# Optimization experiments

Hardware: AMD Instinct MI355X
Metric: run time of the kernel (lower is better)

## Reference

```python
import jax, jax.numpy as jnp
import numpy as np

# Dimensions
B2, T, C = 400, 120, 128          # x: ((B*V), T, C)
V = 25                            # num_point (skeleton joints)
NH_A = 3                          # adjacency heads (A.shape[0])
HEADS, DH = 8, 64                 # attention heads, dim_head
INNER = HEADS * DH                # 512
QKV_C = INNER * 3                 # 1536 = GCN out_channels
EPS = 1e-5                        # torch BatchNorm2d default eps


def setup_inputs() -> dict:
    key = jax.random.key(0)
    ks = jax.random.split(key, 12)
    z = lambda *s: jnp.zeros(s, jnp.float32)
    o = lambda *s: jnp.ones(s, jnp.float32)
    return {
        "x": jax.random.normal(ks[0], (B2, T, C), jnp.float32),
        # GCN shared topology (num_head, V, V)
        "A": jax.random.normal(ks[1], (NH_A, V, V), jnp.float32) * 0.2,
        # per-head 1x1 conv weights/biases (stacked)
        "conv_w": jax.random.normal(ks[2], (NH_A, QKV_C, C), jnp.float32) * 0.02,
        "conv_b": jax.random.normal(ks[3], (NH_A, QKV_C), jnp.float32) * 0.01,
        # main BatchNorm2d (eval mode, running stats)
        "bn_gamma": jax.random.uniform(ks[4], (QKV_C,), jnp.float32, 0.5, 1.5),
        "bn_beta": z(QKV_C),
        "bn_mean": z(QKV_C),
        "bn_var": o(QKV_C),
        # down path: 1x1 conv + BatchNorm2d (in_c != out_c)
        "down_w": jax.random.normal(ks[5], (QKV_C, C), jnp.float32) * 0.02,
        "down_b": z(QKV_C),
        "dbn_gamma": jax.random.uniform(ks[6], (QKV_C,), jnp.float32, 0.5, 1.5),
        "dbn_beta": z(QKV_C),
        "dbn_mean": z(QKV_C),
        "dbn_var": o(QKV_C),
        # to_out Linear(inner_dim -> dim)
        "out_w": jax.random.normal(ks[7], (C, INNER), jnp.float32) * 0.02,
        "out_b": z(C),
    }


def _bn_eval(y, gamma, beta, mean, var):
    # y: (b, o, t, v); BN over channel axis 1, eval mode
    inv = gamma / jnp.sqrt(var + EPS)
    return y * inv[None, :, None, None] + (beta - mean * inv)[None, :, None, None]


def reference(x, A, conv_w, conv_b, bn_gamma, bn_beta, bn_mean, bn_var,
              down_w, down_b, dbn_gamma, dbn_beta, dbn_mean, dbn_var,
              out_w, out_b):
    B = B2 // V
    # '(b v) t c -> b c t v'
    x4 = x.reshape(B, V, T, C).transpose(0, 3, 2, 1)  # (b, c, t, v)

    # ---- GCN projection: sum_h Conv1x1_h(A_h @ x) ----
    z = jnp.einsum('hvu,bctu->bhctv', A, x4)                    # (b,h,c,t,v)
    y = jnp.einsum('hoc,bhctv->botv', conv_w, z)                # (b,O,t,v)
    y = y + conv_b.sum(0)[None, :, None, None]
    y = _bn_eval(y, bn_gamma, bn_beta, bn_mean, bn_var)

    d = jnp.einsum('oc,bctv->botv', down_w, x4) + down_b[None, :, None, None]
    d = _bn_eval(d, dbn_gamma, dbn_beta, dbn_mean, dbn_var)

    y = jax.nn.relu(y + d)                                      # (b,O,t,v)

    # ---- attention over time per (batch*joint) row ----
    qkv = y.transpose(0, 3, 2, 1).reshape(B2, T, QKV_C)         # '(b v) t c'
    q, k, v = jnp.split(qkv, 3, axis=-1)
    split_heads = lambda t: t.reshape(B2, T, HEADS, DH).transpose(0, 2, 1, 3)
    q, k, v = split_heads(q), split_heads(k), split_heads(v)

    dots = jnp.einsum('bhid,bhjd->bhij', q, k) * (DH ** -0.5)
    mask = jnp.tril(jnp.ones((T, T), bool))                     # causal mask
    dots = jnp.where(mask[None, None], dots, -jnp.inf)
    attn = jax.nn.softmax(dots, axis=-1)                        # (B2,H,T,T)

    o = jnp.einsum('bhij,bhjd->bhid', attn, v)
    o = o.transpose(0, 2, 1, 3).reshape(B2, T, INNER)
    out = o @ out_w.T + out_b                                   # (B2,T,C)
    return out, attn
```

## Files before the change

### kernel.cpp

```cpp
#include <hip/hip_runtime.h>


typedef __bf16 bf16;
typedef __bf16 bf16x8 __attribute__((ext_vector_type(8)));
typedef __bf16 bf16x4 __attribute__((ext_vector_type(4)));
typedef float  f32x4  __attribute__((ext_vector_type(4)));
typedef __attribute__((address_space(1))) const void* gptr1;
typedef __attribute__((address_space(3))) void*       lptr3;

#define GLL16(g, l) __builtin_amdgcn_global_load_lds((gptr1)(g), (lptr3)(l), 16, 0, 0)
#define MFMA16(a, b, c) __builtin_amdgcn_mfma_f32_16x16x32_bf16(a, b, c, 0, 0, 0)

__global__ __launch_bounds__(256) void build_weights(
    const float* __restrict__ conv_w, const float* __restrict__ conv_b,
    const float* __restrict__ g1, const float* __restrict__ be1,
    const float* __restrict__ mu1, const float* __restrict__ va1,
    const float* __restrict__ down_w, const float* __restrict__ down_b,
    const float* __restrict__ g2, const float* __restrict__ be2,
    const float* __restrict__ mu2, const float* __restrict__ va2,
    const float* __restrict__ out_w,
    bf16* __restrict__ wcat, bf16* __restrict__ wout, float* __restrict__ bias)
{
    int idx = blockIdx.x * 256 + threadIdx.x;
    if (idx < 1536 * 512) {
        int o = idx >> 9, k = idx & 511;
        float s, w;
        if (k < 384) {
            int h = k >> 7, c = k & 127;
            s = g1[o] * rsqrtf(va1[o] + 1e-5f);
            w = conv_w[(h * 1536 + o) * 128 + c];
        } else {
            s = g2[o] * rsqrtf(va2[o] + 1e-5f);
            w = down_w[o * 128 + (k - 384)];
        }
        wcat[idx] = (bf16)(w * s);
    }
    int i2 = idx - 1536 * 512;
    if (i2 >= 0 && i2 < 128 * 512) wout[i2] = (bf16)out_w[i2];
    int i3 = idx - (1536 * 512 + 128 * 512);
    if (i3 >= 0 && i3 < 1536) {
        int o = i3;
        float s1 = g1[o] * rsqrtf(va1[o] + 1e-5f);
        float s2 = g2[o] * rsqrtf(va2[o] + 1e-5f);
        float cb = conv_b[o] + conv_b[1536 + o] + conv_b[2 * 1536 + o];
        bias[o] = cb * s1 + be1[o] - mu1[o] * s1
                + down_b[o] * s2 + be2[o] - mu2[o] * s2;
    }
}

__global__ __launch_bounds__(256) void transform(
    const float* __restrict__ x, const float* __restrict__ A,
    bf16* __restrict__ zt)
{
    __shared__ float xs[25][128];
    const int tid = threadIdx.x;
    const int bt = blockIdx.x;
    const int b = bt / 120, t = bt - b * 120;
    for (int i = tid; i < 25 * 128; i += 256) {
        int u = i >> 7, c = i & 127;
        xs[u][c] = x[((size_t)(b * 25 + u) * 120 + t) * 128 + c];
    }
    __syncthreads();
    const int c = tid & 127, g = tid >> 7;
    float xr[25];
    #pragma unroll
    for (int u = 0; u < 25; u++) xr[u] = xs[u][c];
    for (int idx = g; idx < 75; idx += 2) {
        int h = idx / 25, v = idx - h * 25;
        const float* Ap = A + (h * 25 + v) * 25;
        float acc = 0.f;
        #pragma unroll
        for (int u = 0; u < 25; u++) acc += Ap[u] * xr[u];
        zt[((size_t)(b * 25 + v) * 120 + t) * 512 + h * 128 + c] = (bf16)acc;
    }
    for (int v = g; v < 25; v += 2)
        zt[((size_t)(b * 25 + v) * 120 + t) * 512 + 384 + c] = (bf16)xs[v][c];
}

__global__ __launch_bounds__(256) void gemm_qkv(
    const bf16* __restrict__ wcat, const bf16* __restrict__ zt,
    const float* __restrict__ bias,
    bf16* __restrict__ qg, bf16* __restrict__ kg, bf16* __restrict__ vtg)
{
    __shared__ __align__(16) char smem[65536];
    const int tid = threadIdx.x, lane = tid & 63, wv = tid >> 6;
    const int wrow = wv >> 1, wcol = wv & 1;
    const int NB = 4500, q8 = NB >> 3, r8 = NB & 7;
    const int xcd = blockIdx.x & 7, sidx = blockIdx.x >> 3;
    const int vid = (xcd < r8 ? xcd * (q8 + 1) : r8 * (q8 + 1) + (xcd - r8) * q8) + sidx;
    const int mt = vid % 12, nt = vid / 12;
    const int colb = lane & 15, rg = lane >> 4;

    f32x4 acc[4][4];
    #pragma unroll
    for (int i = 0; i < 4; i++)
        #pragma unroll
        for (int j = 0; j < 4; j++) acc[i][j] = (f32x4){0.f, 0.f, 0.f, 0.f};

    const char* gA = (const char*)wcat + (size_t)mt * 128 * 1024;
    const char* gB = (const char*)zt + (size_t)nt * 128 * 1024;

    int aoff[4][2], boff[4][2];
    #pragma unroll
    for (int m = 0; m < 4; m++)
        #pragma unroll
        for (int kk = 0; kk < 2; kk++) {
            int swz = (rg * 16 + kk * 64) ^ ((colb & 7) << 4);
            aoff[m][kk] = (wrow * 64 + m * 16 + colb) * 128 + swz;
            boff[m][kk] = (wcol * 64 + m * 16 + colb) * 128 + swz;
        }

    #define STG(kt, bsel) do {                                                  \
        char* As_ = smem + (bsel) * 32768; char* Bs_ = As_ + 16384;             \
        _Pragma("unroll")                                                       \
        for (int j = 0; j < 4; j++) {                                           \
            int c = j * 256 + tid;                                              \
            int r = c >> 3, sl = (c & 7) ^ (r & 7);                             \
            GLL16(gA + (size_t)r * 1024 + (kt) * 128 + sl * 16, As_ + c * 16);  \
            GLL16(gB + (size_t)r * 1024 + (kt) * 128 + sl * 16, Bs_ + c * 16);  \
        } } while (0)

    STG(0, 0);
    asm volatile("s_waitcnt vmcnt(0)" ::: "memory");
    __builtin_amdgcn_s_barrier();
    for (int p = 0; p < 8; p++) {
        const char* As = smem + (p & 1) * 32768;
        const char* Bs = As + 16384;
        if (p < 7) STG(p + 1, (p + 1) & 1);
        bf16x8 af[4][2], bfr[4][2];
        #pragma unroll
        for (int m = 0; m < 4; m++)
            #pragma unroll
            for (int kk = 0; kk < 2; kk++) {
                af[m][kk]  = *(const bf16x8*)(As + aoff[m][kk]);
                bfr[m][kk] = *(const bf16x8*)(Bs + boff[m][kk]);
            }
        __builtin_amdgcn_s_setprio(1);
        #pragma unroll
        for (int m = 0; m < 4; m++)
            #pragma unroll
            for (int n = 0; n < 4; n++)
                #pragma unroll
                for (int kk = 0; kk < 2; kk++)
                    acc[m][n] = MFMA16(af[m][kk], bfr[n][kk], acc[m][n]);
        __builtin_amdgcn_s_setprio(0);
        asm volatile("s_waitcnt vmcnt(0)" ::: "memory");
        __builtin_amdgcn_s_barrier();
    }
    __builtin_amdgcn_sched_barrier(0);

    const int mtb = mt * 128, ntb = nt * 128;
    const int which = mtb >> 9;

    if (which < 2) {
        bf16* Lt = (bf16*)smem;
        const float qs = (which == 0) ? 0.125f : 1.0f;
        #pragma unroll
        for (int m = 0; m < 4; m++) {
            int o0 = wrow * 64 + m * 16 + rg * 4;
            float b0 = bias[mtb + o0 + 0], b1 = bias[mtb + o0 + 1];
            float b2 = bias[mtb + o0 + 2], b3 = bias[mtb + o0 + 3];
            #pragma unroll
            for (int nn = 0; nn < 4; nn++) {
                int n_ = wcol * 64 + nn * 16 + colb;
                bf16x4 pk;
                pk[0] = (bf16)(fmaxf(acc[m][nn][0] + b0, 0.f) * qs);
                pk[1] = (bf16)(fmaxf(acc[m][nn][1] + b1, 0.f) * qs);
                pk[2] = (bf16)(fmaxf(acc[m][nn][2] + b2, 0.f) * qs);
                pk[3] = (bf16)(fmaxf(acc[m][nn][3] + b3, 0.f) * qs);
                *(bf16x4*)((char*)Lt + n_ * 256 + ((o0 * 2) ^ ((n_ & 7) << 4))) = pk;
            }
        }
        __syncthreads();
        bf16* dst = (which == 0) ? qg : kg;
        #pragma unroll
        for (int i = 0; i < 8; i++) {
            int ch = i * 256 + tid;
            int n_ = ch >> 4, c16 = ch & 15;
            int ng = ntb + n_;
            int grp = ng / 120, t = ng - grp * 120;
            int o = mtb + c16 * 8;
            int hd = (o >> 6) & 7, dd0 = o & 63;
            bf16x8 vv = *(const bf16x8*)((const char*)Lt + n_ * 256 +
                                         ((c16 * 16) ^ ((n_ & 7) << 4)));
            *(bf16x8*)(dst + ((size_t)(grp * 8 + hd) * 120 + t) * 64 + dd0) = vv;
        }
    } else {
        #pragma unroll
        for (int m = 0; m < 4; m++) {
            #pragma unroll
            for (int reg = 0; reg < 4; reg++) {
                int o = mtb + wrow * 64 + m * 16 + rg * 4 + reg;
                float bo = bias[o];
                int hd = (o >> 6) & 7, dd = o & 63;
                #pragma unroll
                for (int nn = 0; nn < 4; nn++) {
                    int n = ntb + wcol * 64 + nn * 16 + colb;
                    int grp = n / 120, t = n - grp * 120;
                    float val = fmaxf(acc[m][nn][reg] + bo, 0.f);
                    vtg[((size_t)(grp * 8 + hd) * 64 + dd) * 128 + t] = (bf16)val;
                }
            }
        }
    }
    #undef STG
}

__global__ __launch_bounds__(256) void attn_k(
    const bf16* __restrict__ qg, const bf16* __restrict__ kg,
    const bf16* __restrict__ vtg, float* __restrict__ attn_out,
    bf16* __restrict__ og)
{
    __shared__ __align__(16) char sm[49152];
    char* Vt = sm;
    char* Ks = sm + 16384;
    char* Ps = sm + 16384;
    const int tid = threadIdx.x, lane = tid & 63, wv = tid >> 6;
    const int bh = blockIdx.x;
    const int colb = lane & 15, rg = lane >> 4;

    const char* ksrc = (const char*)kg + (size_t)bh * 15360;
    const char* vsrc = (const char*)vtg + (size_t)bh * 16384;
    #pragma unroll
    for (int is = 0; is < 4; is++) {
        int cb = is * 256 + wv * 64;
        if (cb < 960) {
            int bb = (cb + lane) * 16;
            int row = bb >> 7;
            int gsrc = (bb & ~127) | ((bb & 127) ^ ((row & 7) << 4));
            GLL16(ksrc + gsrc, Ks + cb * 16);
        }
    }
    const char* qsrc = (const char*)qg + (size_t)bh * 15360;
    bf16x8 qf[2][2];
    #pragma unroll
    for (int kk = 0; kk < 2; kk++)
        #pragma unroll
        for (int m = 0; m < 2; m++) {
            int row = wv * 32 + m * 16 + colb;
            qf[kk][m] = *(const bf16x8*)(qsrc + (size_t)row * 128 + rg * 16 + kk * 64);
        }
    #pragma unroll
    for (int is = 0; is < 4; is++) {
        int cb = is * 256 + wv * 64;
        int bb = (cb + lane) * 16;
        int row = bb >> 8;
        int gsrc = (bb & ~255) | ((bb & 255) ^ ((row & 7) << 4));
        GLL16(vsrc + gsrc, Vt + cb * 16);
    }
    asm volatile("s_waitcnt vmcnt(4)" ::: "memory");
    __builtin_amdgcn_s_barrier();
    if (tid < 64) {
        f32x4 z = {0.f, 0.f, 0.f, 0.f};
        int r = 120 + (tid >> 3), off = (tid & 7) * 16;
        *(f32x4*)(Ks + r * 128 + off) = z;
    }
    asm volatile("s_waitcnt lgkmcnt(0)" ::: "memory");
    __builtin_amdgcn_s_barrier();

    f32x4 accs[2][8];
    #pragma unroll
    for (int m = 0; m < 2; m++)
        #pragma unroll
        for (int ct = 0; ct < 8; ct++) accs[m][ct] = (f32x4){0.f, 0.f, 0.f, 0.f};
    #pragma unroll
    for (int kk = 0; kk < 2; kk++) {
        #pragma unroll
        for (int ct = 0; ct < 8; ct++) {
            int rk = ct * 16 + colb;
            int byo = rk * 128 + ((rg * 16 + kk * 64) ^ ((rk & 7) << 4));
            bf16x8 bk = *(const bf16x8*)(Ks + byo);
            accs[0][ct] = MFMA16(qf[kk][0], bk, accs[0][ct]);
            accs[1][ct] = MFMA16(qf[kk][1], bk, accs[1][ct]);
        }
    }
    asm volatile("s_waitcnt vmcnt(0)" ::: "memory");
    __builtin_amdgcn_s_barrier();
    if (tid >= 64 && tid < 128) {
        int d = tid - 64;
        f32x4 z = {0.f, 0.f, 0.f, 0.f};
        *(f32x4*)(Vt + d * 256 + (240 ^ ((d & 7) << 4))) = z;
    }

    const int rqb = wv * 32;
    #pragma unroll
    for (int m = 0; m < 2; m++) {
        #pragma unroll
        for (int reg = 0; reg < 4; reg++) {
            int t_q = rqb + m * 16 + rg * 4 + reg;
            float s[8], mx = -1e30f;
            #pragma unroll
            for (int ct = 0; ct < 8; ct++) {
                int col = ct * 16 + colb;
                bool valid = (col <= t_q) && (col < 120);
                s[ct] = valid ? accs[m][ct][reg] : -1e30f;
                mx = fmaxf(mx, s[ct]);
            }
            #pragma unroll
            for (int d = 1; d < 16; d <<= 1) mx = fmaxf(mx, __shfl_xor(mx, d, 64));
            float p[8], sum = 0.f;
            #pragma unroll
            for (int ct = 0; ct < 8; ct++) {
                p[ct] = (s[ct] > -1e29f) ? __expf(s[ct] - mx) : 0.f;
                sum += p[ct];
            }
            #pragma unroll
            for (int d = 1; d < 16; d <<= 1) sum += __shfl_xor(sum, d, 64);
            float inv = 1.f / sum;
            #pragma unroll
            for (int ct = 0; ct < 8; ct++) {
                int col = ct * 16 + colb;
                int byo = t_q * 256 + ((col * 2) ^ ((t_q & 7) << 4));
                *(bf16*)(Ps + byo) = (bf16)(p[ct] * inv);
            }
        }
    }
    asm volatile("s_waitcnt lgkmcnt(0)" ::: "memory");
    __builtin_amdgcn_s_barrier();

    f32x4 acco[2][4];
    #pragma unroll
    for (int m = 0; m < 2; m++)
        #pragma unroll
        for (int dt = 0; dt < 4; dt++) acco[m][dt] = (f32x4){0.f, 0.f, 0.f, 0.f};
    for (int kk = 0; kk <= wv; kk++) {
        bf16x8 ap[2];
        #pragma unroll
        for (int m = 0; m < 2; m++) {
            int row = rqb + m * 16 + colb;
            int byo = row * 256 + ((rg * 16 + kk * 64) ^ ((row & 7) << 4));
            ap[m] = *(const bf16x8*)(Ps + byo);
        }
        #pragma unroll
        for (int dt = 0; dt < 4; dt++) {
            int rd = dt * 16 + colb;
            int byo = rd * 256 + ((rg * 16 + kk * 64) ^ ((rd & 7) << 4));
            bf16x8 bv = *(const bf16x8*)(Vt + byo);
            acco[0][dt] = MFMA16(ap[0], bv, acco[0][dt]);
            acco[1][dt] = MFMA16(ap[1], bv, acco[1][dt]);
        }
    }

    {
        float* attn_base = attn_out + (size_t)bh * 14400;
        #pragma unroll
        for (int i = 0; i < 15; i++) {
            int chunk = i * 256 + tid;
            if (chunk < 3600) {
                int r = chunk / 30, c4 = chunk - r * 30;
                int byo = r * 256 + ((c4 * 8) ^ ((r & 7) << 4));
                bf16x4 pv4 = *(const bf16x4*)(Ps + byo);
                f32x4 o4 = { (float)pv4[0], (float)pv4[1],
                             (float)pv4[2], (float)pv4[3] };
                *(f32x4*)(attn_base + chunk * 4) = o4;
            }
        }
    }

    const int b2 = bh >> 3, h = bh & 7;
    #pragma unroll
    for (int m = 0; m < 2; m++)
        #pragma unroll
        for (int dt = 0; dt < 4; dt++)
            #pragma unroll
            for (int reg = 0; reg < 4; reg++) {
                int t = rqb + m * 16 + rg * 4 + reg;
                if (t < 120) {
                    int dfull = h * 64 + dt * 16 + colb;
                    og[((size_t)b2 * 120 + t) * 512 + dfull] = (bf16)acco[m][dt][reg];
                }
            }
}

__global__ __launch_bounds__(256) void gemm_out_k(
    const bf16* __restrict__ og, const bf16* __restrict__ wout,
    const float* __restrict__ outb, float* __restrict__ out)
{
    __shared__ __align__(16) char smem[65536];
    const int tid = threadIdx.x, lane = tid & 63, wv = tid >> 6;
    const int wrow = wv >> 1, wcol = wv & 1;
    const int nt = blockIdx.x;
    const int colb = lane & 15, rg = lane >> 4;

    f32x4 acc[4][4];
    #pragma unroll
    for (int i = 0; i < 4; i++)
        #pragma unroll
        for (int j = 0; j < 4; j++) acc[i][j] = (f32x4){0.f, 0.f, 0.f, 0.f};

    const char* gA = (const char*)og + (size_t)nt * 128 * 1024;
    const char* gB = (const char*)wout;

    int aoff[4][2], boff[4][2];
    #pragma unroll
    for (int m = 0; m < 4; m++)
        #pragma unroll
        for (int kk = 0; kk < 2; kk++) {
            int swz = (rg * 16 + kk * 64) ^ ((colb & 7) << 4);
            aoff[m][kk] = (wrow * 64 + m * 16 + colb) * 128 + swz;
            boff[m][kk] = (wcol * 64 + m * 16 + colb) * 128 + swz;
        }

    #define STG_O(kt, bsel) do {                                                \
        char* As_ = smem + (bsel) * 32768; char* Bs_ = As_ + 16384;             \
        _Pragma("unroll")                                                       \
        for (int j = 0; j < 4; j++) {                                           \
            int c = j * 256 + tid;                                              \
            int r = c >> 3, sl = (c & 7) ^ (r & 7);                             \
            GLL16(gA + (size_t)r * 1024 + (kt) * 128 + sl * 16, As_ + c * 16);  \
            GLL16(gB + (size_t)r * 1024 + (kt) * 128 + sl * 16, Bs_ + c * 16);  \
        } } while (0)

    STG_O(0, 0);
    asm volatile("s_waitcnt vmcnt(0)" ::: "memory");
    __builtin_amdgcn_s_barrier();
    for (int p = 0; p < 8; p++) {
        const char* As = smem + (p & 1) * 32768;
        const char* Bs = As + 16384;
        if (p < 7) STG_O(p + 1, (p + 1) & 1);
        bf16x8 af[4][2], bfr[4][2];
        #pragma unroll
        for (int m = 0; m < 4; m++)
            #pragma unroll
            for (int kk = 0; kk < 2; kk++) {
                af[m][kk]  = *(const bf16x8*)(As + aoff[m][kk]);
                bfr[m][kk] = *(const bf16x8*)(Bs + boff[m][kk]);
            }
        __builtin_amdgcn_s_setprio(1);
        #pragma unroll
        for (int m = 0; m < 4; m++)
            #pragma unroll
            for (int n = 0; n < 4; n++)
                #pragma unroll
                for (int kk = 0; kk < 2; kk++)
                    acc[m][n] = MFMA16(af[m][kk], bfr[n][kk], acc[m][n]);
        __builtin_amdgcn_s_setprio(0);
        asm volatile("s_waitcnt vmcnt(0)" ::: "memory");
        __builtin_amdgcn_s_barrier();
    }
    __builtin_amdgcn_sched_barrier(0);

    const int rbase = nt * 128 + wrow * 64;
    #pragma unroll
    for (int m = 0; m < 4; m++)
        #pragma unroll
        for (int reg = 0; reg < 4; reg++) {
            int r = rbase + m * 16 + rg * 4 + reg;
            #pragma unroll
            for (int nn = 0; nn < 4; nn++) {
                int c = wcol * 64 + nn * 16 + colb;
                out[(size_t)r * 128 + c] = acc[m][nn][reg] + outb[c];
            }
        }
    #undef STG_O
}

extern "C" void kernel_launch(void* const* d_in, const int* in_sizes, int n_in,
                              void* d_out, int out_size, void* d_ws, size_t ws_size,
                              hipStream_t stream)
{
    (void)in_sizes; (void)n_in; (void)out_size; (void)ws_size;
    const float* x      = (const float*)d_in[0];
    const float* A      = (const float*)d_in[1];
    const float* conv_w = (const float*)d_in[2];
    const float* conv_b = (const float*)d_in[3];
    const float* bn_g   = (const float*)d_in[4];
    const float* bn_b   = (const float*)d_in[5];
    const float* bn_m   = (const float*)d_in[6];
    const float* bn_v   = (const float*)d_in[7];
    const float* dw     = (const float*)d_in[8];
    const float* db     = (const float*)d_in[9];
    const float* dg     = (const float*)d_in[10];
    const float* dbb    = (const float*)d_in[11];
    const float* dm     = (const float*)d_in[12];
    const float* dvv    = (const float*)d_in[13];
    const float* out_w  = (const float*)d_in[14];
    const float* out_b  = (const float*)d_in[15];

    char* ws = (char*)d_ws;
    const size_t OFF_WCAT = 0;
    const size_t OFF_WOUT = 1572864;
    const size_t OFF_BIAS = 1703936;
    const size_t OFF_ZT   = 1710080;
    const size_t OFF_Q    = 50862080;
    const size_t OFF_K    = 100014080;
    const size_t OFF_VT   = 149166080;
    const size_t OFF_O    = OFF_ZT;

    bf16*  wcat = (bf16*)(ws + OFF_WCAT);
    bf16*  wout = (bf16*)(ws + OFF_WOUT);
    float* bias = (float*)(ws + OFF_BIAS);
    bf16*  zt   = (bf16*)(ws + OFF_ZT);
    bf16*  qg   = (bf16*)(ws + OFF_Q);
    bf16*  kg   = (bf16*)(ws + OFF_K);
    bf16*  vtg  = (bf16*)(ws + OFF_VT);
    bf16*  og   = (bf16*)(ws + OFF_O);
    float* outp = (float*)d_out;
    float* attn = outp + 6144000;

    build_weights<<<3334, 256, 0, stream>>>(conv_w, conv_b, bn_g, bn_b, bn_m, bn_v,
                                            dw, db, dg, dbb, dm, dvv, out_w,
                                            wcat, wout, bias);
    transform<<<1920, 256, 0, stream>>>(x, A, zt);
    gemm_qkv<<<4500, 256, 0, stream>>>(wcat, zt, bias, qg, kg, vtg);
    attn_k<<<3200, 256, 0, stream>>>(qg, kg, vtg, attn, og);
    gemm_out_k<<<375, 256, 0, stream>>>(og, wout, out_b, outp);
}
```

Before: 262.9 us.

## Widen QKV GEMM tile to 128x256 with BK=32 and padded zero rows

```diff
diff --git a/kernel.cpp b/kernel.cpp
--- a/kernel.cpp
+++ b/kernel.cpp
@@ -19,7 +19,8 @@
     const float* __restrict__ g2, const float* __restrict__ be2,
     const float* __restrict__ mu2, const float* __restrict__ va2,
     const float* __restrict__ out_w,
-    bf16* __restrict__ wcat, bf16* __restrict__ wout, float* __restrict__ bias)
+    bf16* __restrict__ wcat, bf16* __restrict__ wout, float* __restrict__ bias,
+    bf16* __restrict__ zt)
 {
     int idx = blockIdx.x * 256 + threadIdx.x;
     if (idx < 1536 * 512) {
@@ -46,6 +47,9 @@
         bias[o] = cb * s1 + be1[o] - mu1[o] * s1
                 + down_b[o] * s2 + be2[o] - mu2[o] * s2;
     }
+    int i4 = idx - (1536 * 512 + 128 * 512 + 1536);
+    if (i4 >= 0 && i4 < 128 * 512)
+        zt[(size_t)48000 * 512 + i4] = (bf16)0.f;
 }
 
 __global__ __launch_bounds__(256) void transform(
@@ -82,128 +86,153 @@
     const float* __restrict__ bias,
     bf16* __restrict__ qg, bf16* __restrict__ kg, bf16* __restrict__ vtg)
 {
-    __shared__ __align__(16) char smem[65536];
+    __shared__ __align__(16) char smem[49152];
     const int tid = threadIdx.x, lane = tid & 63, wv = tid >> 6;
     const int wrow = wv >> 1, wcol = wv & 1;
-    const int NB = 4500, q8 = NB >> 3, r8 = NB & 7;
-    const int xcd = blockIdx.x & 7, sidx = blockIdx.x >> 3;
-    const int vid = (xcd < r8 ? xcd * (q8 + 1) : r8 * (q8 + 1) + (xcd - r8) * q8) + sidx;
-    const int mt = vid % 12, nt = vid / 12;
+    const int vid = (blockIdx.x & 7) * 282 + (blockIdx.x >> 3);
+    const int mt = vid % 12, nt2 = vid / 12;
+    const int mtb = mt * 128, ntb = nt2 * 256;
     const int colb = lane & 15, rg = lane >> 4;
 
-    f32x4 acc[4][4];
+    f32x4 acc0[4][4], acc1[4][4];
     #pragma unroll
     for (int i = 0; i < 4; i++)
         #pragma unroll
-        for (int j = 0; j < 4; j++) acc[i][j] = (f32x4){0.f, 0.f, 0.f, 0.f};
-
-    const char* gA = (const char*)wcat + (size_t)mt * 128 * 1024;
-    const char* gB = (const char*)zt + (size_t)nt * 128 * 1024;
-
-    int aoff[4][2], boff[4][2];
-    #pragma unroll
-    for (int m = 0; m < 4; m++)
-        #pragma unroll
-        for (int kk = 0; kk < 2; kk++) {
-            int swz = (rg * 16 + kk * 64) ^ ((colb & 7) << 4);
-            aoff[m][kk] = (wrow * 64 + m * 16 + colb) * 128 + swz;
-            boff[m][kk] = (wcol * 64 + m * 16 + colb) * 128 + swz;
-        }
+        for (int j = 0; j < 4; j++) {
+            acc0[i][j] = (f32x4){0.f, 0.f, 0.f, 0.f};
+            acc1[i][j] = (f32x4){0.f, 0.f, 0.f, 0.f};
+        }
+
+    const char* gA  = (const char*)wcat + (size_t)mtb * 1024;
+    const char* gB0 = (const char*)zt + (size_t)ntb * 1024;
+    const char* gB1 = (const char*)zt + (size_t)(ntb + 128) * 1024;
+
+    const int rgs = rg ^ ((colb >> 1) & 3);
+    int aoff[4], boff[4];
+    #pragma unroll
+    for (int m = 0; m < 4; m++) {
+        aoff[m] = (wrow * 64 + m * 16 + colb) * 64 + rgs * 16;
+        boff[m] = (wcol * 64 + m * 16 + colb) * 64 + rgs * 16;
+    }
 
     #define STG(kt, bsel) do {                                                  \
-        char* As_ = smem + (bsel) * 32768; char* Bs_ = As_ + 16384;             \
+        char* Bse = smem + (bsel) * 24576;                                      \
         _Pragma("unroll")                                                       \
-        for (int j = 0; j < 4; j++) {                                           \
+        for (int j = 0; j < 2; j++) {                                           \
             int c = j * 256 + tid;                                              \
-            int r = c >> 3, sl = (c & 7) ^ (r & 7);                             \
-            GLL16(gA + (size_t)r * 1024 + (kt) * 128 + sl * 16, As_ + c * 16);  \
-            GLL16(gB + (size_t)r * 1024 + (kt) * 128 + sl * 16, Bs_ + c * 16);  \
+            int r = c >> 2, sl = (c & 3) ^ ((c >> 3) & 3);                      \
+            size_t go = (size_t)r * 1024 + (kt) * 64 + sl * 16;                 \
+            GLL16(gA + go, Bse + c * 16);                                       \
+            GLL16(gB0 + go, Bse + 8192 + c * 16);                               \
+            GLL16(gB1 + go, Bse + 16384 + c * 16);                              \
         } } while (0)
 
     STG(0, 0);
     asm volatile("s_waitcnt vmcnt(0)" ::: "memory");
     __builtin_amdgcn_s_barrier();
-    for (int p = 0; p < 8; p++) {
-        const char* As = smem + (p & 1) * 32768;
-        const char* Bs = As + 16384;
-        if (p < 7) STG(p + 1, (p + 1) & 1);
-        bf16x8 af[4][2], bfr[4][2];
+    for (int p = 0; p < 16; p++) {
+        const char* As  = smem + (p & 1) * 24576;
+        const char* Bs0 = As + 8192;
+        const char* Bs1 = As + 16384;
+        if (p < 15) STG(p + 1, (p + 1) & 1);
+        bf16x8 af[4], bfr[4];
         #pragma unroll
         for (int m = 0; m < 4; m++)
-            #pragma unroll
-            for (int kk = 0; kk < 2; kk++) {
-                af[m][kk]  = *(const bf16x8*)(As + aoff[m][kk]);
-                bfr[m][kk] = *(const bf16x8*)(Bs + boff[m][kk]);
-            }
+            af[m] = *(const bf16x8*)(As + aoff[m]);
+        #pragma unroll
+        for (int n = 0; n < 4; n++)
+            bfr[n] = *(const bf16x8*)(Bs0 + boff[n]);
         __builtin_amdgcn_s_setprio(1);
         #pragma unroll
         for (int m = 0; m < 4; m++)
             #pragma unroll
             for (int n = 0; n < 4; n++)
-                #pragma unroll
-                for (int kk = 0; kk < 2; kk++)
-                    acc[m][n] = MFMA16(af[m][kk], bfr[n][kk], acc[m][n]);
+                acc0[m][n] = MFMA16(af[m], bfr[n], acc0[m][n]);
+        __builtin_amdgcn_s_setprio(0);
+        #pragma unroll
+        for (int n = 0; n < 4; n++)
+            bfr[n] = *(const bf16x8*)(Bs1 + boff[n]);
+        __builtin_amdgcn_s_setprio(1);
+        #pragma unroll
+        for (int m = 0; m < 4; m++)
+            #pragma unroll
+            for (int n = 0; n < 4; n++)
+                acc1[m][n] = MFMA16(af[m], bfr[n], acc1[m][n]);
         __builtin_amdgcn_s_setprio(0);
         asm volatile("s_waitcnt vmcnt(0)" ::: "memory");
         __builtin_amdgcn_s_barrier();
     }
     __builtin_amdgcn_sched_barrier(0);
 
-    const int mtb = mt * 128, ntb = nt * 128;
     const int which = mtb >> 9;
+    const float qs = (which == 0) ? 0.125f : 1.0f;
+
+    #define EPILOGUE_QK(ACC, SUB) do {                                          \
+        bf16* Lt = (bf16*)smem;                    \
+        _Pragma("unroll")                                                       \
+        for (int m = 0; m < 4; m++) {                                           \
+            int o0 = wrow * 64 + m * 16 + rg * 4;                               \
+            float b0 = bias[mtb + o0 + 0], b1 = bias[mtb + o0 + 1];             \
+            float b2 = bias[mtb + o0 + 2], b3 = bias[mtb + o0 + 3];             \
+            _Pragma("unroll")                                                   \
+            for (int nn = 0; nn < 4; nn++) {                                    \
+                int n_ = wcol * 64 + nn * 16 + colb;                            \
+                bf16x4 pk;                                                      \
+                pk[0] = (bf16)(fmaxf(ACC[m][nn][0] + b0, 0.f) * qs);            \
+                pk[1] = (bf16)(fmaxf(ACC[m][nn][1] + b1, 0.f) * qs);            \
+                pk[2] = (bf16)(fmaxf(ACC[m][nn][2] + b2, 0.f) * qs);            \
+                pk[3] = (bf16)(fmaxf(ACC[m][nn][3] + b3, 0.f) * qs);            \
+                *(bf16x4*)((char*)Lt + n_ * 256 + ((o0 * 2) ^ ((n_ & 7) << 4))) = pk; \
+            }                                                                   \
+        }                                                                       \
+        __syncthreads();                                                        \
+        bf16* dst = (which == 0) ? qg : kg;                                     \
+        _Pragma("unroll")                                                       \
+        for (int i = 0; i < 8; i++) {                                           \
+            int ch = i * 256 + tid;                                             \
+            int n_ = ch >> 4, c16 = ch & 15;                                    \
+            int ng = ntb + (SUB) * 128 + n_;                                    \
+            if (ng < 48000) {                                                   \
+                int grp = ng / 120, t = ng - grp * 120;                         \
+                int o = mtb + c16 * 8;                                          \
+                int hd = (o >> 6) & 7, dd0 = o & 63;                            \
+                bf16x8 vv = *(const bf16x8*)((const char*)Lt + n_ * 256 +       \
+                                             ((c16 * 16) ^ ((n_ & 7) << 4)));   \
+                *(bf16x8*)(dst + ((size_t)(grp * 8 + hd) * 120 + t) * 64 + dd0) = vv; \
+            }                                                                   \
+        } } while (0)
+
+    #define EPILOGUE_V(ACC, SUB) do {                                           \
+        _Pragma("unroll")                                                       \
+        for (int m = 0; m < 4; m++) {                                           \
+            _Pragma("unroll")                                                   \
+            for (int reg = 0; reg < 4; reg++) {                                 \
+                int o = mtb + wrow * 64 + m * 16 + rg * 4 + reg;                \
+                float bo = bias[o];                                             \
+                int hd = (o >> 6) & 7, dd = o & 63;                             \
+                _Pragma("unroll")                                               \
+                for (int nn = 0; nn < 4; nn++) {                                \
+                    int n = ntb + (SUB) * 128 + wcol * 64 + nn * 16 + colb;     \
+                    if (n < 48000) {                                            \
+                        int grp = n / 120, t = n - grp * 120;                   \
+                        float val = fmaxf(ACC[m][nn][reg] + bo, 0.f);           \
+                        vtg[((size_t)(grp * 8 + hd) * 64 + dd) * 128 + t] = (bf16)val; \
+                    }                                                           \
+                }                                                               \
+            }                                                                   \
+        } } while (0)
 
     if (which < 2) {
-        bf16* Lt = (bf16*)smem;
-        const float qs = (which == 0) ? 0.125f : 1.0f;
-        #pragma unroll
-        for (int m = 0; m < 4; m++) {
-            int o0 = wrow * 64 + m * 16 + rg * 4;
-            float b0 = bias[mtb + o0 + 0], b1 = bias[mtb + o0 + 1];
-            float b2 = bias[mtb + o0 + 2], b3 = bias[mtb + o0 + 3];
-            #pragma unroll
-            for (int nn = 0; nn < 4; nn++) {
-                int n_ = wcol * 64 + nn * 16 + colb;
-                bf16x4 pk;
-                pk[0] = (bf16)(fmaxf(acc[m][nn][0] + b0, 0.f) * qs);
-                pk[1] = (bf16)(fmaxf(acc[m][nn][1] + b1, 0.f) * qs);
-                pk[2] = (bf16)(fmaxf(acc[m][nn][2] + b2, 0.f) * qs);
-                pk[3] = (bf16)(fmaxf(acc[m][nn][3] + b3, 0.f) * qs);
-                *(bf16x4*)((char*)Lt + n_ * 256 + ((o0 * 2) ^ ((n_ & 7) << 4))) = pk;
-            }
-        }
+        EPILOGUE_QK(acc0, 0);
         __syncthreads();
-        bf16* dst = (which == 0) ? qg : kg;
-        #pragma unroll
-        for (int i = 0; i < 8; i++) {
-            int ch = i * 256 + tid;
-            int n_ = ch >> 4, c16 = ch & 15;
-            int ng = ntb + n_;
-            int grp = ng / 120, t = ng - grp * 120;
-            int o = mtb + c16 * 8;
-            int hd = (o >> 6) & 7, dd0 = o & 63;
-            bf16x8 vv = *(const bf16x8*)((const char*)Lt + n_ * 256 +
-                                         ((c16 * 16) ^ ((n_ & 7) << 4)));
-            *(bf16x8*)(dst + ((size_t)(grp * 8 + hd) * 120 + t) * 64 + dd0) = vv;
-        }
+        EPILOGUE_QK(acc1, 1);
     } else {
-        #pragma unroll
-        for (int m = 0; m < 4; m++) {
-            #pragma unroll
-            for (int reg = 0; reg < 4; reg++) {
-                int o = mtb + wrow * 64 + m * 16 + rg * 4 + reg;
-                float bo = bias[o];
-                int hd = (o >> 6) & 7, dd = o & 63;
-                #pragma unroll
-                for (int nn = 0; nn < 4; nn++) {
-                    int n = ntb + wcol * 64 + nn * 16 + colb;
-                    int grp = n / 120, t = n - grp * 120;
-                    float val = fmaxf(acc[m][nn][reg] + bo, 0.f);
-                    vtg[((size_t)(grp * 8 + hd) * 64 + dd) * 128 + t] = (bf16)val;
-                }
-            }
-        }
+        EPILOGUE_V(acc0, 0);
+        EPILOGUE_V(acc1, 1);
     }
     #undef STG
+    #undef EPILOGUE_QK
+    #undef EPILOGUE_V
 }
 
 __global__ __launch_bounds__(256) void attn_k(
@@ -482,9 +511,9 @@
     const size_t OFF_WOUT = 1572864;
     const size_t OFF_BIAS = 1703936;
     const size_t OFF_ZT   = 1710080;
-    const size_t OFF_Q    = 50862080;
-    const size_t OFF_K    = 100014080;
-    const size_t OFF_VT   = 149166080;
+    const size_t OFF_Q    = 50993152;
+    const size_t OFF_K    = 100145152;
+    const size_t OFF_VT   = 149297152;
     const size_t OFF_O    = OFF_ZT;
 
     bf16*  wcat = (bf16*)(ws + OFF_WCAT);
@@ -498,11 +527,11 @@
     float* outp = (float*)d_out;
     float* attn = outp + 6144000;
 
-    build_weights<<<3334, 256, 0, stream>>>(conv_w, conv_b, bn_g, bn_b, bn_m, bn_v,
+    build_weights<<<3590, 256, 0, stream>>>(conv_w, conv_b, bn_g, bn_b, bn_m, bn_v,
                                             dw, db, dg, dbb, dm, dvv, out_w,
-                                            wcat, wout, bias);
+                                            wcat, wout, bias, zt);
     transform<<<1920, 256, 0, stream>>>(x, A, zt);
-    gemm_qkv<<<4500, 256, 0, stream>>>(wcat, zt, bias, qg, kg, vtg);
+    gemm_qkv<<<2256, 256, 0, stream>>>(wcat, zt, bias, qg, kg, vtg);
     attn_k<<<3200, 256, 0, stream>>>(qg, kg, vtg, attn, og);
     gemm_out_k<<<375, 256, 0, stream>>>(og, wout, out_b, outp);
 }
```

After: 384.5 us. +46.2%, slower.

## Enlarge QKV GEMM tile to 256x128 with 512 threads and triple-buffered K=32 pipeline

Applied to the files above, without the earlier changes.

```diff
diff --git a/kernel.cpp b/kernel.cpp
--- a/kernel.cpp
+++ b/kernel.cpp
@@ -77,18 +77,18 @@
         zt[((size_t)(b * 25 + v) * 120 + t) * 512 + 384 + c] = (bf16)xs[v][c];
 }
 
-__global__ __launch_bounds__(256) void gemm_qkv(
+__global__ __launch_bounds__(512, 4) void gemm_qkv(
     const bf16* __restrict__ wcat, const bf16* __restrict__ zt,
     const float* __restrict__ bias,
     bf16* __restrict__ qg, bf16* __restrict__ kg, bf16* __restrict__ vtg)
 {
-    __shared__ __align__(16) char smem[65536];
+    __shared__ __align__(16) char smem[73728];
     const int tid = threadIdx.x, lane = tid & 63, wv = tid >> 6;
     const int wrow = wv >> 1, wcol = wv & 1;
-    const int NB = 4500, q8 = NB >> 3, r8 = NB & 7;
     const int xcd = blockIdx.x & 7, sidx = blockIdx.x >> 3;
-    const int vid = (xcd < r8 ? xcd * (q8 + 1) : r8 * (q8 + 1) + (xcd - r8) * q8) + sidx;
-    const int mt = vid % 12, nt = vid / 12;
+    const int vid = (xcd < 2 ? xcd * 282 : 564 + (xcd - 2) * 281) + sidx;
+    const int mt = vid % 6, nt = vid / 6;
+    const int mtb = mt * 256, ntb = nt * 128;
     const int colb = lane & 15, rg = lane >> 4;
 
     f32x4 acc[4][4];
@@ -97,60 +97,61 @@
         #pragma unroll
         for (int j = 0; j < 4; j++) acc[i][j] = (f32x4){0.f, 0.f, 0.f, 0.f};
 
-    const char* gA = (const char*)wcat + (size_t)mt * 128 * 1024;
-    const char* gB = (const char*)zt + (size_t)nt * 128 * 1024;
-
-    int aoff[4][2], boff[4][2];
-    #pragma unroll
-    for (int m = 0; m < 4; m++)
-        #pragma unroll
-        for (int kk = 0; kk < 2; kk++) {
-            int swz = (rg * 16 + kk * 64) ^ ((colb & 7) << 4);
-            aoff[m][kk] = (wrow * 64 + m * 16 + colb) * 128 + swz;
-            boff[m][kk] = (wcol * 64 + m * 16 + colb) * 128 + swz;
-        }
+    const char* gA = (const char*)wcat + (size_t)mtb * 1024;
+    const char* gB = (const char*)zt + (size_t)ntb * 1024;
+
+    const int rgs = rg ^ ((colb >> 1) & 3);
+    int aoff[4], boff[4];
+    #pragma unroll
+    for (int m = 0; m < 4; m++) {
+        aoff[m] = (wrow * 64 + m * 16 + colb) * 64 + rgs * 16;
+        boff[m] = (wcol * 64 + m * 16 + colb) * 64 + rgs * 16;
+    }
 
     #define STG(kt, bsel) do {                                                  \
-        char* As_ = smem + (bsel) * 32768; char* Bs_ = As_ + 16384;             \
+        char* As_ = smem + (bsel) * 24576; char* Bs_ = As_ + 16384;             \
         _Pragma("unroll")                                                       \
-        for (int j = 0; j < 4; j++) {                                           \
-            int c = j * 256 + tid;                                              \
-            int r = c >> 3, sl = (c & 7) ^ (r & 7);                             \
-            GLL16(gA + (size_t)r * 1024 + (kt) * 128 + sl * 16, As_ + c * 16);  \
-            GLL16(gB + (size_t)r * 1024 + (kt) * 128 + sl * 16, Bs_ + c * 16);  \
+        for (int j = 0; j < 2; j++) {                                           \
+            int c = j * 512 + tid;                                              \
+            int r = c >> 2, sl = (c & 3) ^ ((c >> 3) & 3);                      \
+            GLL16(gA + (size_t)r * 1024 + (kt) * 64 + sl * 16, As_ + c * 16);   \
+        }                                                                       \
+        {                                                                       \
+            int c = tid;                                                        \
+            int r = c >> 2, sl = (c & 3) ^ ((c >> 3) & 3);                      \
+            GLL16(gB + (size_t)r * 1024 + (kt) * 64 + sl * 16, Bs_ + c * 16);   \
         } } while (0)
 
     STG(0, 0);
+    STG(1, 1);
+    asm volatile("s_waitcnt vmcnt(3)" ::: "memory");
+    __builtin_amdgcn_s_barrier();
+    for (int kt = 0; kt < 16; kt++) {
+        const char* As = smem + (kt % 3) * 24576;
+        const char* Bs = As + 16384;
+        bf16x8 af[4], bfr[4];
+        #pragma unroll
+        for (int m = 0; m < 4; m++) {
+            af[m]  = *(const bf16x8*)(As + aoff[m]);
+            bfr[m] = *(const bf16x8*)(Bs + boff[m]);
+        }
+        int kn = kt + 2;
+        STG(kn < 16 ? kn : 15, kn % 3);
+        __builtin_amdgcn_s_setprio(1);
+        #pragma unroll
+        for (int m = 0; m < 4; m++)
+            #pragma unroll
+            for (int n = 0; n < 4; n++)
+                acc[m][n] = MFMA16(af[m], bfr[n], acc[m][n]);
+        __builtin_amdgcn_s_setprio(0);
+        asm volatile("s_waitcnt vmcnt(3)" ::: "memory");
+        __builtin_amdgcn_s_barrier();
+    }
+    __builtin_amdgcn_sched_barrier(0);
     asm volatile("s_waitcnt vmcnt(0)" ::: "memory");
     __builtin_amdgcn_s_barrier();
-    for (int p = 0; p < 8; p++) {
-        const char* As = smem + (p & 1) * 32768;
-        const char* Bs = As + 16384;
-        if (p < 7) STG(p + 1, (p + 1) & 1);
-        bf16x8 af[4][2], bfr[4][2];
-        #pragma unroll
-        for (int m = 0; m < 4; m++)
-            #pragma unroll
-            for (int kk = 0; kk < 2; kk++) {
-                af[m][kk]  = *(const bf16x8*)(As + aoff[m][kk]);
-                bfr[m][kk] = *(const bf16x8*)(Bs + boff[m][kk]);
-            }
-        __builtin_amdgcn_s_setprio(1);
-        #pragma unroll
-        for (int m = 0; m < 4; m++)
-            #pragma unroll
-            for (int n = 0; n < 4; n++)
-                #pragma unroll
-                for (int kk = 0; kk < 2; kk++)
-                    acc[m][n] = MFMA16(af[m][kk], bfr[n][kk], acc[m][n]);
-        __builtin_amdgcn_s_setprio(0);
-        asm volatile("s_waitcnt vmcnt(0)" ::: "memory");
-        __builtin_amdgcn_s_barrier();
-    }
-    __builtin_amdgcn_sched_barrier(0);
-
-    const int mtb = mt * 128, ntb = nt * 128;
-    const int which = mtb >> 9;
+
+    const int which = mt >> 1;
 
     if (which < 2) {
         bf16* Lt = (bf16*)smem;
@@ -168,20 +169,20 @@
                 pk[1] = (bf16)(fmaxf(acc[m][nn][1] + b1, 0.f) * qs);
                 pk[2] = (bf16)(fmaxf(acc[m][nn][2] + b2, 0.f) * qs);
                 pk[3] = (bf16)(fmaxf(acc[m][nn][3] + b3, 0.f) * qs);
-                *(bf16x4*)((char*)Lt + n_ * 256 + ((o0 * 2) ^ ((n_ & 7) << 4))) = pk;
+                *(bf16x4*)((char*)Lt + n_ * 512 + ((o0 * 2) ^ ((n_ & 7) << 4))) = pk;
             }
         }
         __syncthreads();
         bf16* dst = (which == 0) ? qg : kg;
         #pragma unroll
         for (int i = 0; i < 8; i++) {
-            int ch = i * 256 + tid;
-            int n_ = ch >> 4, c16 = ch & 15;
+            int ch = i * 512 + tid;
+            int n_ = ch >> 5, c16 = ch & 31;
             int ng = ntb + n_;
             int grp = ng / 120, t = ng - grp * 120;
             int o = mtb + c16 * 8;
             int hd = (o >> 6) & 7, dd0 = o & 63;
-            bf16x8 vv = *(const bf16x8*)((const char*)Lt + n_ * 256 +
+            bf16x8 vv = *(const bf16x8*)((const char*)Lt + n_ * 512 +
                                          ((c16 * 16) ^ ((n_ & 7) << 4)));
             *(bf16x8*)(dst + ((size_t)(grp * 8 + hd) * 120 + t) * 64 + dd0) = vv;
         }
@@ -502,7 +503,7 @@
                                             dw, db, dg, dbb, dm, dvv, out_w,
                                             wcat, wout, bias);
     transform<<<1920, 256, 0, stream>>>(x, A, zt);
-    gemm_qkv<<<4500, 256, 0, stream>>>(wcat, zt, bias, qg, kg, vtg);
+    gemm_qkv<<<2250, 512, 0, stream>>>(wcat, zt, bias, qg, kg, vtg);
     attn_k<<<3200, 256, 0, stream>>>(qg, kg, vtg, attn, og);
     gemm_out_k<<<375, 256, 0, stream>>>(og, wout, out_b, outp);
 }
```

Measured after the change: 264.5 us. No clear change (+0.6%).
